# Optimization experiments

Hardware: AMD Instinct MI355X
Metric: run time of the kernel (lower is better)

The kernel has to match this reference:

```python
import jax, jax.numpy as jnp
from jax import lax
import numpy as np

IN_DIM, HID, B, T = 8, 50, 4096, 512

def setup_inputs() -> dict:
    key = jax.random.key(0)
    ks = jax.random.split(key, 8)
    s_ih = 1.0 / np.sqrt(HID)
    return {
        "x": jax.random.normal(ks[0], (B, T, IN_DIM), dtype=jnp.float32),
        "W_ih": jax.random.uniform(ks[1], (3 * HID, IN_DIM), jnp.float32, -s_ih, s_ih),
        "W_hh": jax.random.uniform(ks[2], (3 * HID, HID), jnp.float32, -s_ih, s_ih),
        "b_ih": jax.random.uniform(ks[3], (3 * HID,), jnp.float32, -s_ih, s_ih),
        "b_hh": jax.random.uniform(ks[4], (3 * HID,), jnp.float32, -s_ih, s_ih),
        "W_out": jax.random.uniform(ks[5], (1, HID), jnp.float32, -s_ih, s_ih),
        "b_out": jax.random.uniform(ks[6], (1,), jnp.float32, -s_ih, s_ih),
    }

def reference(x, W_ih, W_hh, b_ih, b_hh, W_out, b_out):
    # Precompute input projections for all timesteps: [B, T, 3H]
    xW = jnp.einsum('bti,gi->btg', x, W_ih) + b_ih

    def step(h, xw_t):  # h: [B, H], xw_t: [B, 3H]
        gi_r, gi_z, gi_n = jnp.split(xw_t, 3, axis=-1)
        gh = h @ W_hh.T + b_hh
        gh_r, gh_z, gh_n = jnp.split(gh, 3, axis=-1)
        r = jax.nn.sigmoid(gi_r + gh_r)
        z = jax.nn.sigmoid(gi_z + gh_z)
        n = jnp.tanh(gi_n + r * gh_n)
        h_new = (1.0 - z) * n + z * h
        return h_new, None

    h0 = jnp.zeros((x.shape[0], W_hh.shape[1]), dtype=x.dtype)
    hT, _ = lax.scan(step, h0, jnp.moveaxis(xW, 1, 0))  # scan over time
    # Linear head on final hidden state; torch squeezes the layer dim -> [B, 1]
    return hT @ W_out.T + b_out
```

## Files before the change

### kernel.cpp

```cpp
#include <hip/hip_runtime.h>

#define HID 50
#define IND 8
#define TLEN 512
#define NB 16
#define CH 128
#define XSTR 1032
#define BSTR 72
#define NTILE 13

typedef _Float16 f16x8 __attribute__((ext_vector_type(8)));
typedef _Float16 f16x4 __attribute__((ext_vector_type(4)));
typedef float f32x4 __attribute__((ext_vector_type(4)));

__device__ __forceinline__ float fast_sigmoid(float v) {
    float e = __builtin_amdgcn_exp2f(-1.44269504f * v);
    return __builtin_amdgcn_rcpf(1.0f + e);
}
__device__ __forceinline__ float fast_tanh(float v) {
    float e = __builtin_amdgcn_exp2f(2.88539008f * v);
    return 1.0f - 2.0f * __builtin_amdgcn_rcpf(e + 1.0f);
}

__global__ __launch_bounds__(832, 1) void gru_mfma6(
    const float* __restrict__ x,
    const float* __restrict__ W_ih,
    const float* __restrict__ W_hh,
    const float* __restrict__ b_ih,
    const float* __restrict__ b_hh,
    const float* __restrict__ W_out,
    const float* __restrict__ b_out,
    float* __restrict__ out)
{
    const int tid  = threadIdx.x;
    const int wave = tid >> 6;
    const int lane = tid & 63;
    const int m16  = lane & 15;
    const int quad = lane >> 4;
    const int bb   = blockIdx.x;
    const int jh   = 4 * wave + quad;

    __shared__ _Float16 x_lds[NB * XSTR];
    __shared__ _Float16 B_lds[2][16 * BSTR];
    __shared__ float    red[NB * 56];

    auto aval = [&](int k) -> float {
        const int R  = 16 * wave + m16;
        const int rj = R >> 2;
        const int g  = R & 3;
        if (rj >= HID) return 0.f;
        if (g <= 1) {
            if (k < HID) return W_hh[(g * HID + rj) * HID + k];
            if (k >= 56) return W_ih[(g * HID + rj) * IND + (k - 56)];
            return 0.f;
        }
        if (g == 2) return (k < HID) ? W_hh[(2 * HID + rj) * HID + k] : 0.f;
        return (k >= 56) ? W_ih[(2 * HID + rj) * IND + (k - 56)] : 0.f;
    };

    f16x8 a0, a1;
#pragma unroll
    for (int j = 0; j < 8; ++j) {
        a0[j] = (_Float16)aval(quad * 8 + j);
        a1[j] = (_Float16)aval(32 + quad * 8 + j);
    }
    f32x4 bias;
#pragma unroll
    for (int r = 0; r < 4; ++r) {
        float v = 0.f;
        if (jh < HID) {
            if (r == 0)      v = b_ih[jh] + b_hh[jh];
            else if (r == 1) v = b_ih[HID + jh] + b_hh[HID + jh];
            else if (r == 2) v = b_hh[2 * HID + jh];
            else             v = b_ih[2 * HID + jh];
        }
        bias[r] = v;
    }
    const f32x4 zero4 = {0.f, 0.f, 0.f, 0.f};
    float h = 0.f;

    auto stage_chunk = [&](int c) {
        if (tid < 512) {
            const int n = tid >> 5;
            const int s = tid & 31;
            const float4* src = (const float4*)(x + ((size_t)(bb * NB + n) * TLEN + (size_t)c * CH) * IND);
#pragma unroll
            for (int r = 0; r < 8; ++r) {
                const int fidx = s + 32 * r;
                const float4 v = src[fidx];
                const int trel = fidx >> 1;
                const int d    = (fidx & 1) * 4;
                *(f16x4*)&x_lds[n * XSTR + trel * 8 + d] =
                    f16x4{(_Float16)v.x, (_Float16)v.y, (_Float16)v.z, (_Float16)v.w};
            }
        }
    };

    for (int idx = tid; idx < 2 * 16 * BSTR; idx += 832)
        B_lds[0][idx] = (_Float16)0.f;
    stage_chunk(0);
    __syncthreads();

    auto step = [&](int t, int cur, int nxt) {
        const f16x8 bf0 = *(const f16x8*)&B_lds[cur][m16 * BSTR + quad * 8];
        const _Float16* bf1p = (quad == 3)
            ? &x_lds[m16 * XSTR + (t & (CH - 1)) * 8]
            : &B_lds[cur][m16 * BSTR + 32 + quad * 8];
        const f16x8 bf1 = *(const f16x8*)bf1p;

        const f32x4 c = __builtin_amdgcn_mfma_f32_16x16x32_f16(a0, bf0, bias,  0, 0, 0);
        const f32x4 d = __builtin_amdgcn_mfma_f32_16x16x32_f16(a1, bf1, zero4, 0, 0, 0);

        const float r  = fast_sigmoid(c[0] + d[0]);
        const float z  = fast_sigmoid(c[1] + d[1]);
        const float nn = fast_tanh((c[3] + d[3]) + r * (c[2] + d[2]));
        h = nn + z * (h - nn);
        if (jh < HID)
            B_lds[nxt][m16 * BSTR + jh] = (_Float16)h;
        __syncthreads();
    };

    for (int t2 = 0; t2 < TLEN; t2 += 2) {
        if ((t2 & (CH - 1)) == 0 && t2 != 0) {
            stage_chunk(t2 >> 7);
            __syncthreads();
        }
        step(t2,     0, 1);
        step(t2 + 1, 1, 0);
    }

    if (jh < HID)
        red[m16 * 56 + jh] = h * W_out[jh];
    __syncthreads();
    if (tid < NB) {
        float s = b_out[0];
        for (int j = 0; j < HID; ++j) s += red[tid * 56 + j];
        out[bb * NB + tid] = s;
    }
}

extern "C" void kernel_launch(void* const* d_in, const int* in_sizes, int n_in,
                              void* d_out, int out_size, void* d_ws, size_t ws_size,
                              hipStream_t stream) {
    const float* x     = (const float*)d_in[0];
    const float* W_ih  = (const float*)d_in[1];
    const float* W_hh  = (const float*)d_in[2];
    const float* b_ih  = (const float*)d_in[3];
    const float* b_hh  = (const float*)d_in[4];
    const float* W_out = (const float*)d_in[5];
    const float* b_out = (const float*)d_in[6];
    float* out = (float*)d_out;

    const int B = in_sizes[0] / (TLEN * IND);
    gru_mfma6<<<B / NB, 832, 0, stream>>>(x, W_ih, W_hh, b_ih, b_hh, W_out, b_out, out);
}
```

Baseline: 264.4 us.

## Assign two MFMA row tiles per wave, shrinking block from 13 to 7 waves

Each wave now computes two 16-row gate tiles instead of one, so the workgroup drops from 13 waves (832 threads) to 7 (448 threads). Fewer waves take part in the per-timestep __syncthreads barrier, which is meant to cut synchronization cost in the serial recurrence. In exchange each wave issues four MFMAs and two gate-activation chains per step, which lengthens its critical path. Chunk staging of x is rewritten as a strided loop over all threads.

```diff
diff --git a/kernel.cpp b/kernel.cpp
--- a/kernel.cpp
+++ b/kernel.cpp
@@ -7,7 +7,7 @@
 #define CH 128
 #define XSTR 1032
 #define BSTR 72
-#define NTILE 13
+#define NWAVE 7
 
 typedef _Float16 f16x8 __attribute__((ext_vector_type(8)));
 typedef _Float16 f16x4 __attribute__((ext_vector_type(4)));
@@ -22,7 +22,7 @@
     return 1.0f - 2.0f * __builtin_amdgcn_rcpf(e + 1.0f);
 }
 
-__global__ __launch_bounds__(832, 1) void gru_mfma6(
+__global__ __launch_bounds__(NWAVE * 64, 1) void gru_mfma7(
     const float* __restrict__ x,
     const float* __restrict__ W_ih,
     const float* __restrict__ W_hh,
@@ -38,14 +38,19 @@
     const int m16  = lane & 15;
     const int quad = lane >> 4;
     const int bb   = blockIdx.x;
-    const int jh   = 4 * wave + quad;
+
+    const int T0 = 2 * wave;
+    const int T1 = 2 * wave + 1;
+    const bool has1 = (T1 <= 12);
+    const int jh0 = 4 * T0 + quad;
+    const int jh1 = 4 * T1 + quad;
 
     __shared__ _Float16 x_lds[NB * XSTR];
     __shared__ _Float16 B_lds[2][16 * BSTR];
     __shared__ float    red[NB * 56];
 
-    auto aval = [&](int k) -> float {
-        const int R  = 16 * wave + m16;
+    auto aval = [&](int T, int k) -> float {
+        const int R  = 16 * T + m16;
         const int rj = R >> 2;
         const int g  = R & 3;
         if (rj >= HID) return 0.f;
@@ -57,46 +62,45 @@
         if (g == 2) return (k < HID) ? W_hh[(2 * HID + rj) * HID + k] : 0.f;
         return (k >= 56) ? W_ih[(2 * HID + rj) * IND + (k - 56)] : 0.f;
     };
+    auto bval = [&](int jh, int r) -> float {
+        if (jh >= HID) return 0.f;
+        if (r == 0) return b_ih[jh] + b_hh[jh];
+        if (r == 1) return b_ih[HID + jh] + b_hh[HID + jh];
+        if (r == 2) return b_hh[2 * HID + jh];
+        return b_ih[2 * HID + jh];
+    };
 
-    f16x8 a0, a1;
+    f16x8 a0[2], a1[2];
+    f32x4 bias[2];
 #pragma unroll
     for (int j = 0; j < 8; ++j) {
-        a0[j] = (_Float16)aval(quad * 8 + j);
-        a1[j] = (_Float16)aval(32 + quad * 8 + j);
+        a0[0][j] = (_Float16)aval(T0, quad * 8 + j);
+        a1[0][j] = (_Float16)aval(T0, 32 + quad * 8 + j);
+        a0[1][j] = has1 ? (_Float16)aval(T1, quad * 8 + j)      : (_Float16)0.f;
+        a1[1][j] = has1 ? (_Float16)aval(T1, 32 + quad * 8 + j) : (_Float16)0.f;
     }
-    f32x4 bias;
 #pragma unroll
     for (int r = 0; r < 4; ++r) {
-        float v = 0.f;
-        if (jh < HID) {
-            if (r == 0)      v = b_ih[jh] + b_hh[jh];
-            else if (r == 1) v = b_ih[HID + jh] + b_hh[HID + jh];
-            else if (r == 2) v = b_hh[2 * HID + jh];
-            else             v = b_ih[2 * HID + jh];
-        }
-        bias[r] = v;
+        bias[0][r] = bval(jh0, r);
+        bias[1][r] = has1 ? bval(jh1, r) : 0.f;
     }
     const f32x4 zero4 = {0.f, 0.f, 0.f, 0.f};
-    float h = 0.f;
+    float h0 = 0.f, h1 = 0.f;
 
     auto stage_chunk = [&](int c) {
-        if (tid < 512) {
-            const int n = tid >> 5;
-            const int s = tid & 31;
-            const float4* src = (const float4*)(x + ((size_t)(bb * NB + n) * TLEN + (size_t)c * CH) * IND);
-#pragma unroll
-            for (int r = 0; r < 8; ++r) {
-                const int fidx = s + 32 * r;
-                const float4 v = src[fidx];
-                const int trel = fidx >> 1;
-                const int d    = (fidx & 1) * 4;
-                *(f16x4*)&x_lds[n * XSTR + trel * 8 + d] =
-                    f16x4{(_Float16)v.x, (_Float16)v.y, (_Float16)v.z, (_Float16)v.w};
-            }
+        const float* xbase = x + (size_t)(bb * NB) * TLEN * IND + (size_t)c * CH * IND;
+        for (int f = tid; f < NB * (CH * IND / 4); f += NWAVE * 64) {
+            const int n    = f >> 8;
+            const int fidx = f & 255;
+            const float4 v = ((const float4*)(xbase + (size_t)n * TLEN * IND))[fidx];
+            const int trel = fidx >> 1;
+            const int d    = (fidx & 1) * 4;
+            *(f16x4*)&x_lds[n * XSTR + trel * 8 + d] =
+                f16x4{(_Float16)v.x, (_Float16)v.y, (_Float16)v.z, (_Float16)v.w};
         }
     };
 
-    for (int idx = tid; idx < 2 * 16 * BSTR; idx += 832)
+    for (int idx = tid; idx < 2 * 16 * BSTR; idx += NWAVE * 64)
         B_lds[0][idx] = (_Float16)0.f;
     stage_chunk(0);
     __syncthreads();
@@ -108,15 +112,27 @@
             : &B_lds[cur][m16 * BSTR + 32 + quad * 8];
         const f16x8 bf1 = *(const f16x8*)bf1p;
 
-        const f32x4 c = __builtin_amdgcn_mfma_f32_16x16x32_f16(a0, bf0, bias,  0, 0, 0);
-        const f32x4 d = __builtin_amdgcn_mfma_f32_16x16x32_f16(a1, bf1, zero4, 0, 0, 0);
+        const f32x4 c0 = __builtin_amdgcn_mfma_f32_16x16x32_f16(a0[0], bf0, bias[0], 0, 0, 0);
+        const f32x4 d0 = __builtin_amdgcn_mfma_f32_16x16x32_f16(a1[0], bf1, zero4,   0, 0, 0);
+        const f32x4 c1 = __builtin_amdgcn_mfma_f32_16x16x32_f16(a0[1], bf0, bias[1], 0, 0, 0);
+        const f32x4 d1 = __builtin_amdgcn_mfma_f32_16x16x32_f16(a1[1], bf1, zero4,   0, 0, 0);
 
-        const float r  = fast_sigmoid(c[0] + d[0]);
-        const float z  = fast_sigmoid(c[1] + d[1]);
-        const float nn = fast_tanh((c[3] + d[3]) + r * (c[2] + d[2]));
-        h = nn + z * (h - nn);
-        if (jh < HID)
-            B_lds[nxt][m16 * BSTR + jh] = (_Float16)h;
+        {
+            const float r  = fast_sigmoid(c0[0] + d0[0]);
+            const float z  = fast_sigmoid(c0[1] + d0[1]);
+            const float nn = fast_tanh((c0[3] + d0[3]) + r * (c0[2] + d0[2]));
+            h0 = nn + z * (h0 - nn);
+            if (jh0 < HID)
+                B_lds[nxt][m16 * BSTR + jh0] = (_Float16)h0;
+        }
+        if (has1) {
+            const float r  = fast_sigmoid(c1[0] + d1[0]);
+            const float z  = fast_sigmoid(c1[1] + d1[1]);
+            const float nn = fast_tanh((c1[3] + d1[3]) + r * (c1[2] + d1[2]));
+            h1 = nn + z * (h1 - nn);
+            if (jh1 < HID)
+                B_lds[nxt][m16 * BSTR + jh1] = (_Float16)h1;
+        }
         __syncthreads();
     };
 
@@ -129,8 +145,8 @@
         step(t2 + 1, 1, 0);
     }
 
-    if (jh < HID)
-        red[m16 * 56 + jh] = h * W_out[jh];
+    if (jh0 < HID) red[m16 * 56 + jh0] = h0 * W_out[jh0];
+    if (has1 && jh1 < HID) red[m16 * 56 + jh1] = h1 * W_out[jh1];
     __syncthreads();
     if (tid < NB) {
         float s = b_out[0];
@@ -152,5 +168,5 @@
     float* out = (float*)d_out;
 
     const int B = in_sizes[0] / (TLEN * IND);
-    gru_mfma6<<<B / NB, 832, 0, stream>>>(x, W_ih, W_hh, b_ih, b_hh, W_out, b_out, out);
+    gru_mfma7<<<B / NB, NWAVE * 64, 0, stream>>>(x, W_ih, W_hh, b_ih, b_hh, W_out, b_out, out);
 }
```

Measured after the change: 299.5 us. 13.3% more time.
